# Optimization experiments

Hardware: AMD Instinct MI355X
Metric: run time of the kernel (lower is better)

## Reference

```python
import jax, jax.numpy as jnp
import numpy as np

N = 50000          # nodes
E = 1600000        # edges (avg degree 32)
B = 64             # graphs in batch
D_NODE = 128
D_EDGE = 64
D_EMB = 128
D_HID = 2 * D_EMB  # GCN output channels
EPS = 1e-5


def setup_inputs() -> dict:
    key = jax.random.key(0)
    ks = jax.random.split(key, 12)
    g = lambda k, shape: jax.random.normal(k, shape, jnp.float32) * (shape[0] ** -0.5)
    return {
        "x": jax.random.normal(ks[0], (N, D_NODE), jnp.float32),
        "edge_attr": jax.random.normal(ks[1], (E, D_EDGE), jnp.float32),
        "edge_index": jax.random.randint(ks[2], (2, E), 0, N),
        "batch": jnp.sort(jax.random.randint(ks[3], (N,), 0, B)),
        # GCNConv params
        "W1": g(ks[4], (D_NODE, D_HID)), "b1": jnp.zeros((D_HID,), jnp.float32),
        # TransformerConv params (heads=1)
        "Wq": g(ks[5], (D_HID, D_EMB)), "bq": jnp.zeros((D_EMB,), jnp.float32),
        "Wk": g(ks[6], (D_HID, D_EMB)), "bk": jnp.zeros((D_EMB,), jnp.float32),
        "Wv": g(ks[7], (D_HID, D_EMB)), "bv": jnp.zeros((D_EMB,), jnp.float32),
        "We": g(ks[8], (D_EDGE, D_EMB)), "be": jnp.zeros((D_EMB,), jnp.float32),
        "Wr": g(ks[9], (D_HID, D_EMB)), "br": jnp.zeros((D_EMB,), jnp.float32),
        # LayerNorm params
        "gamma": jnp.ones((D_EMB,), jnp.float32), "beta": jnp.zeros((D_EMB,), jnp.float32),
    }


def _forward(x, edge_attr, edge_index, batch,
             W1, b1, Wq, bq, Wk, bk, Wv, bv, We, be, Wr, br, gamma, beta):
    src, dst = edge_index[0], edge_index[1]

    # ---- GCNConv: symmetric normalization with self-loops ----
    xw = x @ W1                                                # [N, D_HID]
    deg = 1.0 + jax.ops.segment_sum(jnp.ones((E,), x.dtype), dst, num_segments=N)
    dinv = jax.lax.rsqrt(deg)                                  # deg >= 1
    norm = dinv[src] * dinv[dst]                               # [E]
    agg = jax.ops.segment_sum(xw[src] * norm[:, None], dst, num_segments=N)
    h = agg + xw * (dinv * dinv)[:, None] + b1                 # self-loop term
    h = jax.nn.relu(h)                                         # dropout = identity (eval)

    # ---- TransformerConv (heads=1, edge_dim) ----
    q = h @ Wq + bq                                            # [N, D_EMB]
    k = h @ Wk + bk
    v = h @ Wv + bv
    e = edge_attr @ We + be                                    # [E, D_EMB]
    k_j = k[src] + e
    v_j = v[src] + e
    logits = jnp.sum(q[dst] * k_j, axis=-1) / jnp.sqrt(jnp.float32(D_EMB))  # [E]
    # segment softmax over incoming edges of each target node
    lmax = jax.ops.segment_max(logits, dst, num_segments=N)
    exp_l = jnp.exp(logits - lmax[dst])
    denom = jax.ops.segment_sum(exp_l, dst, num_segments=N)
    alpha = exp_l / denom[dst]                                 # [E]
    out = jax.ops.segment_sum(alpha[:, None] * v_j, dst, num_segments=N)
    out = out + h @ Wr + br                                    # root/skip connection

    # ---- LayerNorm + ReLU ----
    mu = jnp.mean(out, axis=-1, keepdims=True)
    var = jnp.var(out, axis=-1, keepdims=True)
    out = (out - mu) * jax.lax.rsqrt(var + EPS) * gamma + beta
    out = jax.nn.relu(out)

    # ---- global mean pool over graphs ----
    sums = jax.ops.segment_sum(out, batch, num_segments=B)     # [B, D_EMB]
    cnts = jax.ops.segment_sum(jnp.ones((N,), out.dtype), batch, num_segments=B)
    return sums / jnp.maximum(cnts, 1.0)[:, None]


def reference(x, edge_attr, edge_index, batch,
              W1, b1, Wq, bq, Wk, bk, Wv, bv, We, be, Wr, br, gamma, beta):
    return _forward(x, edge_attr, edge_index, batch,
                    W1, b1, Wq, bq, Wk, bk, Wv, bv, We, be, Wr, br, gamma, beta)
```

## Files before the change

### kernel.cpp

```cpp
#include <hip/hip_runtime.h>

typedef short bf16x8 __attribute__((ext_vector_type(8)));
typedef float f32x4 __attribute__((ext_vector_type(4)));

#define DN 128
#define DE 64
#define DEMB 128
#define DHID 256
#define SCALE 0.08838834764831845f

__device__ __forceinline__ ushort f2bf(float f) {
  unsigned u = __float_as_uint(f);
  return (ushort)((u + 0x7FFFu + ((u >> 16) & 1u)) >> 16);
}
__device__ __forceinline__ float bf2f(ushort u) {
  return __uint_as_float((unsigned)u << 16);
}

__global__ void k_prep1(const float* __restrict__ W1, ushort* __restrict__ Wp1) {
  int idx = blockIdx.x * 256 + threadIdx.x;
  if (idx >= 16 * 4 * 64 * 8) return;
  int j = idx & 7, lane = (idx >> 3) & 63, s = (idx >> 9) & 3, t = idx >> 11;
  int k = s * 32 + (lane >> 4) * 8 + j;
  int c = t * 16 + (lane & 15);
  Wp1[idx] = f2bf(W1[k * DHID + c]);
}

__global__ void k_prep2(const float* __restrict__ Wq, const float* __restrict__ Wk,
                        const float* __restrict__ Wv, const float* __restrict__ Wr,
                        const float* __restrict__ We, ushort* __restrict__ Wp2) {
  int idx = blockIdx.x * 256 + threadIdx.x;
  if (idx >= 36 * 8 * 64 * 8) return;
  int j = idx & 7, lane = (idx >> 3) & 63, s = (idx >> 9) & 7, t = idx >> 12;
  int k = s * 32 + (lane >> 4) * 8 + j;
  int c = t * 16 + (lane & 15);
  float v;
  if (c < 128)       v = Wq[k * DEMB + c] * SCALE;
  else if (c < 256)  v = Wk[k * DEMB + (c - 128)];
  else if (c < 384)  v = Wv[k * DEMB + (c - 256)];
  else if (c < 512)  v = Wr[k * DEMB + (c - 384)];
  else {
    int cc = c - 512;
    float a = 0.f;
    for (int u = 0; u < DEMB; ++u) a += Wq[k * DEMB + u] * We[cc * DEMB + u];
    v = a * SCALE;
  }
  Wp2[idx] = f2bf(v);
}

__global__ void k_prep_b(const float* __restrict__ bq, const float* __restrict__ bk,
                         const float* __restrict__ bv, const float* __restrict__ br,
                         const float* __restrict__ be, const float* __restrict__ We,
                         float* __restrict__ bcat) {
  int j = blockIdx.x * 256 + threadIdx.x;
  if (j >= 576) return;
  float v;
  if (j < 128)       v = bq[j] * SCALE;
  else if (j < 256)  v = bk[j - 128] + be[j - 128];
  else if (j < 384)  v = bv[j - 256] + be[j - 256];
  else if (j < 512)  v = br[j - 384];
  else {
    int cc = j - 512;
    float a = 0.f;
    for (int u = 0; u < DEMB; ++u) a += bq[u] * We[cc * DEMB + u];
    v = a * SCALE;
  }
  bcat[j] = v;
}

__global__ void k_prep3(const float* __restrict__ We, ushort* __restrict__ Wp3) {
  int idx = blockIdx.x * 256 + threadIdx.x;
  if (idx >= 8 * 2 * 64 * 8) return;
  int j = idx & 7, lane = (idx >> 3) & 63, s = (idx >> 9) & 1, t = idx >> 10;
  int k = s * 32 + (lane >> 4) * 8 + j;
  int c = t * 16 + (lane & 15);
  Wp3[idx] = f2bf(We[k * DEMB + c]);
}

__global__ void k_deg(const int* __restrict__ ei, int* __restrict__ degi, int nE) {
  int e = blockIdx.x * 256 + threadIdx.x;
  if (e < nE) atomicAdd(&degi[ei[nE + e]], 1);
}

__global__ void k_dinv(const int* __restrict__ degi, float* __restrict__ dinv, int nN) {
  int n = blockIdx.x * 256 + threadIdx.x;
  if (n < nN) dinv[n] = rsqrtf(1.0f + (float)degi[n]);
}

__global__ __launch_bounds__(1024) void k_scan(const int* __restrict__ degi,
                                               int* __restrict__ row_ptr, int n) {
  __shared__ int wsum[16];
  __shared__ int carry_s;
  int lane = threadIdx.x & 63, wid = threadIdx.x >> 6;
  if (threadIdx.x == 0) carry_s = 0;
  __syncthreads();
  for (int base = 0; base < n; base += 1024) {
    int i = base + threadIdx.x;
    int v = (i < n) ? degi[i] : 0;
    int sc = v;
    #pragma unroll
    for (int off = 1; off < 64; off <<= 1) {
      int t = __shfl_up(sc, off);
      if (lane >= off) sc += t;
    }
    if (lane == 63) wsum[wid] = sc;
    int carry0 = carry_s;
    __syncthreads();
    if (wid == 0) {
      int w = (lane < 16) ? wsum[lane] : 0;
      int swc = w;
      #pragma unroll
      for (int off = 1; off < 16; off <<= 1) {
        int t = __shfl_up(swc, off);
        if (lane >= off) swc += t;
      }
      if (lane < 16) wsum[lane] = swc - w;
      if (lane == 15) carry_s = carry0 + swc;
    }
    __syncthreads();
    if (i < n) row_ptr[i] = carry0 + wsum[wid] + sc - v;
    __syncthreads();
  }
  if (threadIdx.x == 0) row_ptr[n] = carry_s;
}

__global__ void k_scatter(const int* __restrict__ ei, const int* __restrict__ row_ptr,
                          int* __restrict__ cursor, int2* __restrict__ csr_se, int nE) {
  int e = blockIdx.x * 256 + threadIdx.x;
  if (e >= nE) return;
  int dst = ei[nE + e];
  int pos = row_ptr[dst] + atomicAdd(&cursor[dst], 1);
  csr_se[pos] = make_int2(ei[e], e);
}

__global__ void k_gbounds(const int* __restrict__ batch, int* __restrict__ gstart,
                          int nN, int B) {
  int n = blockIdx.x * 256 + threadIdx.x;
  if (n >= nN) return;
  int b = batch[n];
  if (n == 0) {
    for (int g = 0; g <= b; ++g) gstart[g] = 0;
  } else {
    int pb = batch[n - 1];
    for (int g = pb + 1; g <= b; ++g) gstart[g] = n;
  }
  if (n == nN - 1) {
    for (int g = b + 1; g <= B; ++g) gstart[g] = nN;
  }
}

__global__ __launch_bounds__(256) void k_xcast(const float* __restrict__ x,
                                               const float* __restrict__ dinv,
                                               ushort* __restrict__ xsb, int nN) {
  int idx = blockIdx.x * 256 + threadIdx.x;
  if (idx >= nN * 32) return;
  int n = idx >> 5, q = idx & 31;
  float dn = dinv[n];
  float4 v = *(const float4*)&x[(size_t)n * DN + q * 4];
  ushort4 o;
  o.x = f2bf(v.x * dn); o.y = f2bf(v.y * dn);
  o.z = f2bf(v.z * dn); o.w = f2bf(v.w * dn);
  *(ushort4*)&xsb[(size_t)n * DN + q * 4] = o;
}

__global__ __launch_bounds__(256) void k_gcnX(const ushort* __restrict__ xsb,
                                              const int2* __restrict__ csr_se,
                                              const int* __restrict__ row_ptr,
                                              const float* __restrict__ dinv,
                                              ushort* __restrict__ aggxb, int nN) {
  int lane = threadIdx.x & 63;
  int n = blockIdx.x * 4 + (threadIdx.x >> 6);
  if (n >= nN) return;
  int grp = lane >> 4, l15 = lane & 15;
  int beg = row_ptr[n], end = row_ptr[n + 1];
  float acc[8] = {};
  for (int i0 = beg; i0 < end; i0 += 16) {
    #pragma unroll
    for (int u = 0; u < 4; ++u) {
      int e = i0 + u * 4 + grp;
      bool val = e < end;
      int cl = val ? e : end - 1;
      int src = csr_se[cl].x;
      uint4 xa = *(const uint4*)&xsb[(size_t)src * DN + l15 * 8];
      float w = val ? 1.f : 0.f;
      unsigned qq[4] = {xa.x, xa.y, xa.z, xa.w};
      #pragma unroll
      for (int d = 0; d < 4; ++d) {
        acc[2*d]   = fmaf(w, __uint_as_float(qq[d] << 16), acc[2*d]);
        acc[2*d+1] = fmaf(w, __uint_as_float(qq[d] & 0xFFFF0000u), acc[2*d+1]);
      }
    }
  }
  #pragma unroll
  for (int d = 0; d < 8; ++d) {
    acc[d] += __shfl_xor(acc[d], 16);
    acc[d] += __shfl_xor(acc[d], 32);
  }
  if (grp == 0) {
    uint4 sa = *(const uint4*)&xsb[(size_t)n * DN + l15 * 8];
    unsigned sq[4] = {sa.x, sa.y, sa.z, sa.w};
    float dn = dinv[n];
    ushort o[8];
    #pragma unroll
    for (int d = 0; d < 4; ++d) {
      float lo = __uint_as_float(sq[d] << 16);
      float hi = __uint_as_float(sq[d] & 0xFFFF0000u);
      o[2*d]   = f2bf(dn * (acc[2*d]   + lo));
      o[2*d+1] = f2bf(dn * (acc[2*d+1] + hi));
    }
    uint4 ov = {(unsigned)o[0] | ((unsigned)o[1] << 16),
                (unsigned)o[2] | ((unsigned)o[3] << 16),
                (unsigned)o[4] | ((unsigned)o[5] << 16),
                (unsigned)o[6] | ((unsigned)o[7] << 16)};
    *(uint4*)&aggxb[(size_t)n * DN + l15 * 8] = ov;
  }
}

__global__ __launch_bounds__(256) void k_gemm1b(const ushort* __restrict__ aggxb,
                                                const ushort* __restrict__ Wp1,
                                                const float* __restrict__ b1,
                                                ushort* __restrict__ hb, int nN) {
  int lane = threadIdx.x & 63, wave = threadIdx.x >> 6;
  int l15 = lane & 15, lh = lane >> 4;
  int m0 = blockIdx.x * 16;
  int rowa = m0 + l15; if (rowa >= nN) rowa = nN - 1;
  f32x4 acc[4] = {};
  #pragma unroll
  for (int s = 0; s < 4; ++s) {
    bf16x8 af = *(const bf16x8*)&aggxb[(size_t)rowa * DN + s * 32 + lh * 8];
    #pragma unroll
    for (int tt = 0; tt < 4; ++tt) {
      int t = wave * 4 + tt;
      bf16x8 bf = *(const bf16x8*)&Wp1[((t * 4 + s) * 64 + lane) * 8];
      acc[tt] = __builtin_amdgcn_mfma_f32_16x16x32_bf16(af, bf, acc[tt], 0, 0, 0);
    }
  }
  #pragma unroll
  for (int tt = 0; tt < 4; ++tt) {
    int c = (wave * 4 + tt) * 16 + l15;
    float bc = b1[c];
    #pragma unroll
    for (int r = 0; r < 4; ++r) {
      int row = m0 + lh * 4 + r;
      if (row < nN) hb[(size_t)row * DHID + c] = f2bf(fmaxf(acc[tt][r] + bc, 0.f));
    }
  }
}

__global__ __launch_bounds__(256) void k_gemm2(const ushort* __restrict__ hb,
                                               const ushort* __restrict__ Wp2,
                                               const float* __restrict__ bcat,
                                               ushort* __restrict__ qwb,
                                               ushort* __restrict__ kb,
                                               ushort* __restrict__ vb,
                                               ushort* __restrict__ hrb, int nN) {
  int lane = threadIdx.x & 63, wave = threadIdx.x >> 6;
  int l15 = lane & 15, lh = lane >> 4;
  int m0 = blockIdx.x * 16;
  int rowa = m0 + l15; if (rowa >= nN) rowa = nN - 1;
  f32x4 acc[9] = {};
  for (int s = 0; s < 8; ++s) {
    bf16x8 af = *(const bf16x8*)&hb[(size_t)rowa * DHID + s * 32 + lh * 8];
    #pragma unroll
    for (int tt = 0; tt < 9; ++tt) {
      int t = wave * 9 + tt;
      bf16x8 bf = *(const bf16x8*)&Wp2[((t * 8 + s) * 64 + lane) * 8];
      acc[tt] = __builtin_amdgcn_mfma_f32_16x16x32_bf16(af, bf, acc[tt], 0, 0, 0);
    }
  }
  #pragma unroll
  for (int tt = 0; tt < 9; ++tt) {
    int c = (wave * 9 + tt) * 16 + l15;
    float bc = bcat[c];
    #pragma unroll
    for (int r = 0; r < 4; ++r) {
      int row = m0 + lh * 4 + r;
      if (row >= nN) continue;
      ushort val = f2bf(acc[tt][r] + bc);
      if (c < 128)      qwb[(size_t)row * 192 + c] = val;
      else if (c < 256) kb[(size_t)row * 128 + (c - 128)] = val;
      else if (c < 384) vb[(size_t)row * 128 + (c - 256)] = val;
      else if (c < 512) hrb[(size_t)row * 128 + (c - 384)] = val;
      else              qwb[(size_t)row * 192 + 128 + (c - 512)] = val;
    }
  }
}

__global__ __launch_bounds__(256) void k_edge(const ushort* __restrict__ qwb,
                                              const ushort* __restrict__ kb,
                                              const ushort* __restrict__ vb,
                                              const float* __restrict__ ea32,
                                              const int2* __restrict__ csr_se,
                                              const int* __restrict__ row_ptr,
                                              float* __restrict__ sden,
                                              float* __restrict__ vaccf,
                                              ushort* __restrict__ ewb, int nN) {
  int lane = threadIdx.x & 63;
  int n = blockIdx.x * 4 + (threadIdx.x >> 6);
  if (n >= nN) return;
  int grp = lane >> 4, l15 = lane & 15;
  const ushort* qp = &qwb[(size_t)n * 192];
  bf16x8 qv = *(const bf16x8*)&qp[l15 * 8];
  ushort4 wv = *(const ushort4*)&qp[128 + l15 * 4];
  float q[8];
  #pragma unroll
  for (int d = 0; d < 8; ++d) q[d] = bf2f((ushort)qv[d]);
  float w0 = bf2f(wv.x), w1 = bf2f(wv.y), w2 = bf2f(wv.z), w3 = bf2f(wv.w);
  float s_acc = 0.f;
  float av[8] = {};
  float ae[4] = {};
  int beg = row_ptr[n], end = row_ptr[n + 1];
  for (int i0 = beg; i0 < end; i0 += 16) {
    int2 se[4]; bool vl[4];
    #pragma unroll
    for (int u = 0; u < 4; ++u) {
      int e = i0 + u * 4 + grp;
      vl[u] = e < end;
      se[u] = csr_se[vl[u] ? e : end - 1];
    }
    bf16x8 kv8[4]; bf16x8 vv8[4]; float4 eav[4];
    #pragma unroll
    for (int u = 0; u < 4; ++u) {
      kv8[u] = *(const bf16x8*)&kb[(size_t)se[u].x * 128 + l15 * 8];
      vv8[u] = *(const bf16x8*)&vb[(size_t)se[u].x * 128 + l15 * 8];
      eav[u] = *(const float4*)&ea32[(size_t)se[u].y * DE + l15 * 4];
    }
    #pragma unroll
    for (int u = 0; u < 4; ++u) {
      float dot = w0 * eav[u].x + w1 * eav[u].y + w2 * eav[u].z + w3 * eav[u].w;
      #pragma unroll
      for (int d = 0; d < 8; ++d) dot = fmaf(q[d], bf2f((ushort)kv8[u][d]), dot);
      dot += __shfl_xor(dot, 1);
      dot += __shfl_xor(dot, 2);
      dot += __shfl_xor(dot, 4);
      dot += __shfl_xor(dot, 8);
      float p = vl[u] ? __expf(dot) : 0.f;
      s_acc += p;
      #pragma unroll
      for (int d = 0; d < 8; ++d) av[d] = fmaf(p, bf2f((ushort)vv8[u][d]), av[d]);
      ae[0] = fmaf(p, eav[u].x, ae[0]);
      ae[1] = fmaf(p, eav[u].y, ae[1]);
      ae[2] = fmaf(p, eav[u].z, ae[2]);
      ae[3] = fmaf(p, eav[u].w, ae[3]);
    }
  }
  s_acc += __shfl_xor(s_acc, 16); s_acc += __shfl_xor(s_acc, 32);
  #pragma unroll
  for (int d = 0; d < 8; ++d) {
    av[d] += __shfl_xor(av[d], 16);
    av[d] += __shfl_xor(av[d], 32);
  }
  #pragma unroll
  for (int d = 0; d < 4; ++d) {
    ae[d] += __shfl_xor(ae[d], 16);
    ae[d] += __shfl_xor(ae[d], 32);
  }
  if (grp == 0) {
    if (l15 == 0) sden[n] = s_acc;
    float4 o0 = {av[0], av[1], av[2], av[3]};
    float4 o1 = {av[4], av[5], av[6], av[7]};
    float* vr = &vaccf[(size_t)n * 128 + l15 * 8];
    *(float4*)vr = o0;
    *(float4*)(vr + 4) = o1;
    ushort4 eo;
    eo.x = f2bf(ae[0]); eo.y = f2bf(ae[1]); eo.z = f2bf(ae[2]); eo.w = f2bf(ae[3]);
    *(ushort4*)&ewb[(size_t)n * DE + l15 * 4] = eo;
  }
}

__global__ __launch_bounds__(256) void k_ewe(const ushort* __restrict__ ewb,
                                             const ushort* __restrict__ Wp3,
                                             float* __restrict__ ewout, int nN) {
  int lane = threadIdx.x & 63, wave = threadIdx.x >> 6;
  int l15 = lane & 15, lh = lane >> 4;
  int m0 = blockIdx.x * 16;
  int rowa = m0 + l15; if (rowa >= nN) rowa = nN - 1;
  f32x4 acc[2] = {};
  #pragma unroll
  for (int s = 0; s < 2; ++s) {
    bf16x8 af = *(const bf16x8*)&ewb[(size_t)rowa * DE + s * 32 + lh * 8];
    #pragma unroll
    for (int tt = 0; tt < 2; ++tt) {
      int t = wave * 2 + tt;
      bf16x8 bf = *(const bf16x8*)&Wp3[((t * 2 + s) * 64 + lane) * 8];
      acc[tt] = __builtin_amdgcn_mfma_f32_16x16x32_bf16(af, bf, acc[tt], 0, 0, 0);
    }
  }
  #pragma unroll
  for (int tt = 0; tt < 2; ++tt) {
    int c = (wave * 2 + tt) * 16 + l15;
    #pragma unroll
    for (int r = 0; r < 4; ++r) {
      int row = m0 + lh * 4 + r;
      if (row < nN) ewout[(size_t)row * 128 + c] = acc[tt][r];
    }
  }
}

__global__ __launch_bounds__(256) void k_fin(const float* __restrict__ sden,
                                             const float* __restrict__ vaccf,
                                             const float* __restrict__ ewout,
                                             const ushort* __restrict__ hrb,
                                             const float* __restrict__ gamma,
                                             const float* __restrict__ beta,
                                             float* __restrict__ ynorm, int nN) {
  int lane = threadIdx.x & 63, grp = lane >> 5, l5 = lane & 31;
  int n = blockIdx.x * 8 + (threadIdx.x >> 6) * 2 + grp;
  if (n >= nN) return;
  float s = sden[n];
  float inv = (s > 0.f) ? 1.f / s : 0.f;
  float4 v4 = *(const float4*)&vaccf[(size_t)n * 128 + l5 * 4];
  float4 w4 = *(const float4*)&ewout[(size_t)n * 128 + l5 * 4];
  ushort4 hv = *(const ushort4*)&hrb[(size_t)n * 128 + l5 * 4];
  float4 o4;
  o4.x = (v4.x + w4.x) * inv + bf2f(hv.x);
  o4.y = (v4.y + w4.y) * inv + bf2f(hv.y);
  o4.z = (v4.z + w4.z) * inv + bf2f(hv.z);
  o4.w = (v4.w + w4.w) * inv + bf2f(hv.w);
  float s1 = o4.x + o4.y + o4.z + o4.w;
  float sq = o4.x*o4.x + o4.y*o4.y + o4.z*o4.z + o4.w*o4.w;
  #pragma unroll
  for (int off = 1; off < 32; off <<= 1) {
    s1 += __shfl_xor(s1, off);
    sq += __shfl_xor(sq, off);
  }
  float mu = s1 * (1.f / 128.f);
  float var = sq * (1.f / 128.f) - mu * mu;
  float rstd = rsqrtf(var + 1e-5f);
  float4 g4 = *(const float4*)&gamma[l5 * 4];
  float4 b4 = *(const float4*)&beta[l5 * 4];
  float4 y;
  y.x = fmaxf((o4.x - mu) * rstd * g4.x + b4.x, 0.f);
  y.y = fmaxf((o4.y - mu) * rstd * g4.y + b4.y, 0.f);
  y.z = fmaxf((o4.z - mu) * rstd * g4.z + b4.z, 0.f);
  y.w = fmaxf((o4.w - mu) * rstd * g4.w + b4.w, 0.f);
  *(float4*)&ynorm[(size_t)n * 128 + l5 * 4] = y;
}

__global__ __launch_bounds__(128) void k_pool(const float* __restrict__ ynorm,
                                              const int* __restrict__ gstart,
                                              float* __restrict__ out) {
  int b = blockIdx.x, t = threadIdx.x;
  int beg = gstart[b], end = gstart[b + 1];
  float a0 = 0.f, a1 = 0.f, a2 = 0.f, a3 = 0.f;
  int n = beg;
  for (; n + 4 <= end; n += 4) {
    a0 += ynorm[(size_t)(n + 0) * 128 + t];
    a1 += ynorm[(size_t)(n + 1) * 128 + t];
    a2 += ynorm[(size_t)(n + 2) * 128 + t];
    a3 += ynorm[(size_t)(n + 3) * 128 + t];
  }
  for (; n < end; ++n) a0 += ynorm[(size_t)n * 128 + t];
  float acc = (a0 + a1) + (a2 + a3);
  out[b * 128 + t] = acc / fmaxf((float)(end - beg), 1.f);
}

extern "C" void kernel_launch(void* const* d_in, const int* in_sizes, int n_in,
                              void* d_out, int out_size, void* d_ws, size_t ws_size,
                              hipStream_t stream) {
  const float* x         = (const float*)d_in[0];
  const float* edge_attr = (const float*)d_in[1];
  const int*   edge_index= (const int*)d_in[2];
  const int*   batch     = (const int*)d_in[3];
  const float* W1 = (const float*)d_in[4];
  const float* b1 = (const float*)d_in[5];
  const float* Wq = (const float*)d_in[6];  const float* bq = (const float*)d_in[7];
  const float* Wk = (const float*)d_in[8];  const float* bk = (const float*)d_in[9];
  const float* Wv = (const float*)d_in[10]; const float* bv = (const float*)d_in[11];
  const float* We = (const float*)d_in[12]; const float* be = (const float*)d_in[13];
  const float* Wr = (const float*)d_in[14]; const float* br = (const float*)d_in[15];
  const float* gamma = (const float*)d_in[16];
  const float* beta  = (const float*)d_in[17];
  float* out = (float*)d_out;

  const int nN = in_sizes[0] / DN;
  const int nE = in_sizes[1] / DE;
  const int B  = out_size / DEMB;

  char* p = (char*)d_ws;
  auto alloc = [&](size_t bytes) -> void* {
    void* r = (void*)p;
    p += (bytes + 255) & ~(size_t)255;
    return r;
  };
  int*   degi   = (int*)  alloc((size_t)nN * 4);
  int*   cursor = (int*)  alloc((size_t)nN * 4);
  size_t zero_bytes = (size_t)(p - (char*)d_ws);
  int*    row_ptr = (int*)   alloc((size_t)(nN + 1) * 4);
  int*    gstart  = (int*)   alloc((size_t)(B + 1) * 4);
  float*  dinv    = (float*) alloc((size_t)nN * 4);
  int2*   csr_se  = (int2*)  alloc((size_t)nE * 8);
  ushort* Wp1     = (ushort*)alloc((size_t)16 * 4 * 64 * 8 * 2);
  ushort* Wp2     = (ushort*)alloc((size_t)36 * 8 * 64 * 8 * 2);
  ushort* Wp3     = (ushort*)alloc((size_t)8 * 2 * 64 * 8 * 2);
  float*  bcat    = (float*) alloc(576 * 4);
  ushort* qwb     = (ushort*)alloc((size_t)nN * 192 * 2);
  ushort* hrb     = (ushort*)alloc((size_t)nN * 128 * 2);
  ushort* hb      = (ushort*)alloc((size_t)nN * DHID * 2);
  ushort* xsb     = (ushort*)alloc((size_t)nN * DN * 2);
  ushort* aggxb   = (ushort*)alloc((size_t)nN * DN * 2);
  ushort* kb      = xsb;
  ushort* vb      = aggxb;
  float*  sden    = (float*) alloc((size_t)nN * 4);
  float*  vaccf   = (float*) alloc((size_t)nN * 128 * 4);
  ushort* ewb     = (ushort*)alloc((size_t)nN * DE * 2);
  float*  ewout   = (float*) alloc((size_t)nN * 128 * 4);
  float*  ynorm   = (float*) alloc((size_t)nN * 128 * 4);
  size_t required = (size_t)(p - (char*)d_ws);
  if (ws_size < required) return;

  hipMemsetAsync(d_ws, 0, zero_bytes, stream);

  k_prep1<<<128, 256, 0, stream>>>(W1, Wp1);
  k_prep2<<<576, 256, 0, stream>>>(Wq, Wk, Wv, Wr, We, Wp2);
  k_prep_b<<<3, 256, 0, stream>>>(bq, bk, bv, br, be, We, bcat);
  k_prep3<<<32, 256, 0, stream>>>(We, Wp3);
  k_deg<<<(nE + 255) / 256, 256, 0, stream>>>(edge_index, degi, nE);
  k_dinv<<<(nN + 255) / 256, 256, 0, stream>>>(degi, dinv, nN);
  k_scan<<<1, 1024, 0, stream>>>(degi, row_ptr, nN);
  k_scatter<<<(nE + 255) / 256, 256, 0, stream>>>(edge_index, row_ptr, cursor,
                                                  csr_se, nE);
  k_gbounds<<<(nN + 255) / 256, 256, 0, stream>>>(batch, gstart, nN, B);
  k_xcast<<<(nN * 32 + 255) / 256, 256, 0, stream>>>(x, dinv, xsb, nN);
  k_gcnX<<<(nN + 3) / 4, 256, 0, stream>>>(xsb, csr_se, row_ptr, dinv, aggxb, nN);
  k_gemm1b<<<(nN + 15) / 16, 256, 0, stream>>>(aggxb, Wp1, b1, hb, nN);
  k_gemm2<<<(nN + 15) / 16, 256, 0, stream>>>(hb, Wp2, bcat, qwb, kb, vb, hrb, nN);
  k_edge<<<(nN + 3) / 4, 256, 0, stream>>>(qwb, kb, vb, edge_attr, csr_se, row_ptr,
                                           sden, vaccf, ewb, nN);
  k_ewe<<<(nN + 15) / 16, 256, 0, stream>>>(ewb, Wp3, ewout, nN);
  k_fin<<<(nN + 7) / 8, 256, 0, stream>>>(sden, vaccf, ewout, hrb, gamma, beta,
                                          ynorm, nN);
  k_pool<<<B, 128, 0, stream>>>(ynorm, gstart, out);
}
```

Before: 661.2 us.

## Merge prep/dinv/gbounds kernels and deepen gather batching in gcnX and edge

Folds the four weight-prep kernels into one launch, computes dinv inside the scan kernel, and moves graph-boundary detection into the x-cast kernel, cutting five launches. The GCN aggregation now loads 8 neighbour rows per iteration instead of 4, and the attention edge kernel loads 6 instead of 4, with a launch-bounds occupancy hint. The aim is to reduce launch overhead and expose more memory-level parallelism in the gathers, at the cost of higher register pressure and more wasted lanes on low-degree nodes.

```diff
diff --git a/kernel.cpp b/kernel.cpp
--- a/kernel.cpp
+++ b/kernel.cpp
@@ -17,64 +17,60 @@
   return __uint_as_float((unsigned)u << 16);
 }
 
-__global__ void k_prep1(const float* __restrict__ W1, ushort* __restrict__ Wp1) {
-  int idx = blockIdx.x * 256 + threadIdx.x;
-  if (idx >= 16 * 4 * 64 * 8) return;
-  int j = idx & 7, lane = (idx >> 3) & 63, s = (idx >> 9) & 3, t = idx >> 11;
-  int k = s * 32 + (lane >> 4) * 8 + j;
-  int c = t * 16 + (lane & 15);
-  Wp1[idx] = f2bf(W1[k * DHID + c]);
-}
-
-__global__ void k_prep2(const float* __restrict__ Wq, const float* __restrict__ Wk,
-                        const float* __restrict__ Wv, const float* __restrict__ Wr,
-                        const float* __restrict__ We, ushort* __restrict__ Wp2) {
-  int idx = blockIdx.x * 256 + threadIdx.x;
-  if (idx >= 36 * 8 * 64 * 8) return;
-  int j = idx & 7, lane = (idx >> 3) & 63, s = (idx >> 9) & 7, t = idx >> 12;
-  int k = s * 32 + (lane >> 4) * 8 + j;
-  int c = t * 16 + (lane & 15);
-  float v;
-  if (c < 128)       v = Wq[k * DEMB + c] * SCALE;
-  else if (c < 256)  v = Wk[k * DEMB + (c - 128)];
-  else if (c < 384)  v = Wv[k * DEMB + (c - 256)];
-  else if (c < 512)  v = Wr[k * DEMB + (c - 384)];
-  else {
-    int cc = c - 512;
-    float a = 0.f;
-    for (int u = 0; u < DEMB; ++u) a += Wq[k * DEMB + u] * We[cc * DEMB + u];
-    v = a * SCALE;
-  }
-  Wp2[idx] = f2bf(v);
-}
-
-__global__ void k_prep_b(const float* __restrict__ bq, const float* __restrict__ bk,
-                         const float* __restrict__ bv, const float* __restrict__ br,
-                         const float* __restrict__ be, const float* __restrict__ We,
-                         float* __restrict__ bcat) {
-  int j = blockIdx.x * 256 + threadIdx.x;
-  if (j >= 576) return;
-  float v;
-  if (j < 128)       v = bq[j] * SCALE;
-  else if (j < 256)  v = bk[j - 128] + be[j - 128];
-  else if (j < 384)  v = bv[j - 256] + be[j - 256];
-  else if (j < 512)  v = br[j - 384];
-  else {
-    int cc = j - 512;
-    float a = 0.f;
-    for (int u = 0; u < DEMB; ++u) a += bq[u] * We[cc * DEMB + u];
-    v = a * SCALE;
-  }
-  bcat[j] = v;
-}
-
-__global__ void k_prep3(const float* __restrict__ We, ushort* __restrict__ Wp3) {
-  int idx = blockIdx.x * 256 + threadIdx.x;
-  if (idx >= 8 * 2 * 64 * 8) return;
-  int j = idx & 7, lane = (idx >> 3) & 63, s = (idx >> 9) & 1, t = idx >> 10;
-  int k = s * 32 + (lane >> 4) * 8 + j;
-  int c = t * 16 + (lane & 15);
-  Wp3[idx] = f2bf(We[k * DEMB + c]);
+__global__ void k_prep_all(const float* __restrict__ W1, const float* __restrict__ Wq,
+                           const float* __restrict__ Wk, const float* __restrict__ Wv,
+                           const float* __restrict__ Wr, const float* __restrict__ We,
+                           const float* __restrict__ bq, const float* __restrict__ bk,
+                           const float* __restrict__ bv, const float* __restrict__ br,
+                           const float* __restrict__ be,
+                           ushort* __restrict__ Wp1, ushort* __restrict__ Wp2,
+                           ushort* __restrict__ Wp3, float* __restrict__ bcat) {
+  int bid = blockIdx.x;
+  if (bid < 576) {
+    int idx = bid * 256 + threadIdx.x;
+    int j = idx & 7, lane = (idx >> 3) & 63, s = (idx >> 9) & 7, t = idx >> 12;
+    int k = s * 32 + (lane >> 4) * 8 + j;
+    int c = t * 16 + (lane & 15);
+    float v;
+    if (c < 128)       v = Wq[k * DEMB + c] * SCALE;
+    else if (c < 256)  v = Wk[k * DEMB + (c - 128)];
+    else if (c < 384)  v = Wv[k * DEMB + (c - 256)];
+    else if (c < 512)  v = Wr[k * DEMB + (c - 384)];
+    else {
+      int cc = c - 512;
+      float a = 0.f;
+      for (int u = 0; u < DEMB; ++u) a += Wq[k * DEMB + u] * We[cc * DEMB + u];
+      v = a * SCALE;
+    }
+    Wp2[idx] = f2bf(v);
+  } else if (bid < 704) {
+    int idx = (bid - 576) * 256 + threadIdx.x;
+    int j = idx & 7, lane = (idx >> 3) & 63, s = (idx >> 9) & 3, t = idx >> 11;
+    int k = s * 32 + (lane >> 4) * 8 + j;
+    int c = t * 16 + (lane & 15);
+    Wp1[idx] = f2bf(W1[k * DHID + c]);
+  } else if (bid < 736) {
+    int idx = (bid - 704) * 256 + threadIdx.x;
+    int j = idx & 7, lane = (idx >> 3) & 63, s = (idx >> 9) & 1, t = idx >> 10;
+    int k = s * 32 + (lane >> 4) * 8 + j;
+    int c = t * 16 + (lane & 15);
+    Wp3[idx] = f2bf(We[k * DEMB + c]);
+  } else {
+    int j = (bid - 736) * 256 + threadIdx.x;
+    if (j >= 576) return;
+    float v;
+    if (j < 128)       v = bq[j] * SCALE;
+    else if (j < 256)  v = bk[j - 128] + be[j - 128];
+    else if (j < 384)  v = bv[j - 256] + be[j - 256];
+    else if (j < 512)  v = br[j - 384];
+    else {
+      int cc = j - 512;
+      float a = 0.f;
+      for (int u = 0; u < DEMB; ++u) a += bq[u] * We[cc * DEMB + u];
+      v = a * SCALE;
+    }
+    bcat[j] = v;
+  }
 }
 
 __global__ void k_deg(const int* __restrict__ ei, int* __restrict__ degi, int nE) {
@@ -82,13 +78,9 @@
   if (e < nE) atomicAdd(&degi[ei[nE + e]], 1);
 }
 
-__global__ void k_dinv(const int* __restrict__ degi, float* __restrict__ dinv, int nN) {
-  int n = blockIdx.x * 256 + threadIdx.x;
-  if (n < nN) dinv[n] = rsqrtf(1.0f + (float)degi[n]);
-}
-
 __global__ __launch_bounds__(1024) void k_scan(const int* __restrict__ degi,
-                                               int* __restrict__ row_ptr, int n) {
+                                               int* __restrict__ row_ptr,
+                                               float* __restrict__ dinv, int n) {
   __shared__ int wsum[16];
   __shared__ int carry_s;
   int lane = threadIdx.x & 63, wid = threadIdx.x >> 6;
@@ -97,6 +89,7 @@
   for (int base = 0; base < n; base += 1024) {
     int i = base + threadIdx.x;
     int v = (i < n) ? degi[i] : 0;
+    if (i < n) dinv[i] = rsqrtf(1.0f + (float)v);
     int sc = v;
     #pragma unroll
     for (int off = 1; off < 64; off <<= 1) {
@@ -133,34 +126,33 @@
   csr_se[pos] = make_int2(ei[e], e);
 }
 
-__global__ void k_gbounds(const int* __restrict__ batch, int* __restrict__ gstart,
-                          int nN, int B) {
-  int n = blockIdx.x * 256 + threadIdx.x;
-  if (n >= nN) return;
-  int b = batch[n];
-  if (n == 0) {
-    for (int g = 0; g <= b; ++g) gstart[g] = 0;
-  } else {
-    int pb = batch[n - 1];
-    for (int g = pb + 1; g <= b; ++g) gstart[g] = n;
-  }
-  if (n == nN - 1) {
-    for (int g = b + 1; g <= B; ++g) gstart[g] = nN;
-  }
-}
-
 __global__ __launch_bounds__(256) void k_xcast(const float* __restrict__ x,
                                                const float* __restrict__ dinv,
-                                               ushort* __restrict__ xsb, int nN) {
+                                               const int* __restrict__ batch,
+                                               int* __restrict__ gstart,
+                                               ushort* __restrict__ xsb, int nN, int B) {
   int idx = blockIdx.x * 256 + threadIdx.x;
-  if (idx >= nN * 32) return;
-  int n = idx >> 5, q = idx & 31;
-  float dn = dinv[n];
-  float4 v = *(const float4*)&x[(size_t)n * DN + q * 4];
-  ushort4 o;
-  o.x = f2bf(v.x * dn); o.y = f2bf(v.y * dn);
-  o.z = f2bf(v.z * dn); o.w = f2bf(v.w * dn);
-  *(ushort4*)&xsb[(size_t)n * DN + q * 4] = o;
+  if (idx < nN) {
+    int b = batch[idx];
+    if (idx == 0) {
+      for (int g = 0; g <= b; ++g) gstart[g] = 0;
+    } else {
+      int pb = batch[idx - 1];
+      for (int g = pb + 1; g <= b; ++g) gstart[g] = idx;
+    }
+    if (idx == nN - 1) {
+      for (int g = b + 1; g <= B; ++g) gstart[g] = nN;
+    }
+  }
+  if (idx < nN * 32) {
+    int n = idx >> 5, q = idx & 31;
+    float dn = dinv[n];
+    float4 v = *(const float4*)&x[(size_t)n * DN + q * 4];
+    ushort4 o;
+    o.x = f2bf(v.x * dn); o.y = f2bf(v.y * dn);
+    o.z = f2bf(v.z * dn); o.w = f2bf(v.w * dn);
+    *(ushort4*)&xsb[(size_t)n * DN + q * 4] = o;
+  }
 }
 
 __global__ __launch_bounds__(256) void k_gcnX(const ushort* __restrict__ xsb,
@@ -174,16 +166,22 @@
   int grp = lane >> 4, l15 = lane & 15;
   int beg = row_ptr[n], end = row_ptr[n + 1];
   float acc[8] = {};
-  for (int i0 = beg; i0 < end; i0 += 16) {
-    #pragma unroll
-    for (int u = 0; u < 4; ++u) {
+  for (int i0 = beg; i0 < end; i0 += 32) {
+    int src[8]; bool vl[8];
+    #pragma unroll
+    for (int u = 0; u < 8; ++u) {
       int e = i0 + u * 4 + grp;
-      bool val = e < end;
-      int cl = val ? e : end - 1;
-      int src = csr_se[cl].x;
-      uint4 xa = *(const uint4*)&xsb[(size_t)src * DN + l15 * 8];
-      float w = val ? 1.f : 0.f;
-      unsigned qq[4] = {xa.x, xa.y, xa.z, xa.w};
+      vl[u] = e < end;
+      src[u] = csr_se[vl[u] ? e : end - 1].x;
+    }
+    uint4 xa[8];
+    #pragma unroll
+    for (int u = 0; u < 8; ++u)
+      xa[u] = *(const uint4*)&xsb[(size_t)src[u] * DN + l15 * 8];
+    #pragma unroll
+    for (int u = 0; u < 8; ++u) {
+      float w = vl[u] ? 1.f : 0.f;
+      unsigned qq[4] = {xa[u].x, xa[u].y, xa[u].z, xa[u].w};
       #pragma unroll
       for (int d = 0; d < 4; ++d) {
         acc[2*d]   = fmaf(w, __uint_as_float(qq[d] << 16), acc[2*d]);
@@ -286,15 +284,15 @@
   }
 }
 
-__global__ __launch_bounds__(256) void k_edge(const ushort* __restrict__ qwb,
-                                              const ushort* __restrict__ kb,
-                                              const ushort* __restrict__ vb,
-                                              const float* __restrict__ ea32,
-                                              const int2* __restrict__ csr_se,
-                                              const int* __restrict__ row_ptr,
-                                              float* __restrict__ sden,
-                                              float* __restrict__ vaccf,
-                                              ushort* __restrict__ ewb, int nN) {
+__global__ __launch_bounds__(256, 4) void k_edge(const ushort* __restrict__ qwb,
+                                                 const ushort* __restrict__ kb,
+                                                 const ushort* __restrict__ vb,
+                                                 const float* __restrict__ ea32,
+                                                 const int2* __restrict__ csr_se,
+                                                 const int* __restrict__ row_ptr,
+                                                 float* __restrict__ sden,
+                                                 float* __restrict__ vaccf,
+                                                 ushort* __restrict__ ewb, int nN) {
   int lane = threadIdx.x & 63;
   int n = blockIdx.x * 4 + (threadIdx.x >> 6);
   if (n >= nN) return;
@@ -310,23 +308,23 @@
   float av[8] = {};
   float ae[4] = {};
   int beg = row_ptr[n], end = row_ptr[n + 1];
-  for (int i0 = beg; i0 < end; i0 += 16) {
-    int2 se[4]; bool vl[4];
-    #pragma unroll
-    for (int u = 0; u < 4; ++u) {
+  for (int i0 = beg; i0 < end; i0 += 24) {
+    int2 se[6]; bool vl[6];
+    #pragma unroll
+    for (int u = 0; u < 6; ++u) {
       int e = i0 + u * 4 + grp;
       vl[u] = e < end;
       se[u] = csr_se[vl[u] ? e : end - 1];
     }
-    bf16x8 kv8[4]; bf16x8 vv8[4]; float4 eav[4];
-    #pragma unroll
-    for (int u = 0; u < 4; ++u) {
+    bf16x8 kv8[6]; bf16x8 vv8[6]; float4 eav[6];
+    #pragma unroll
+    for (int u = 0; u < 6; ++u) {
       kv8[u] = *(const bf16x8*)&kb[(size_t)se[u].x * 128 + l15 * 8];
       vv8[u] = *(const bf16x8*)&vb[(size_t)se[u].x * 128 + l15 * 8];
       eav[u] = *(const float4*)&ea32[(size_t)se[u].y * DE + l15 * 4];
     }
     #pragma unroll
-    for (int u = 0; u < 4; ++u) {
+    for (int u = 0; u < 6; ++u) {
       float dot = w0 * eav[u].x + w1 * eav[u].y + w2 * eav[u].z + w3 * eav[u].w;
       #pragma unroll
       for (int d = 0; d < 8; ++d) dot = fmaf(q[d], bf2f((ushort)kv8[u][d]), dot);
@@ -511,17 +509,14 @@
 
   hipMemsetAsync(d_ws, 0, zero_bytes, stream);
 
-  k_prep1<<<128, 256, 0, stream>>>(W1, Wp1);
-  k_prep2<<<576, 256, 0, stream>>>(Wq, Wk, Wv, Wr, We, Wp2);
-  k_prep_b<<<3, 256, 0, stream>>>(bq, bk, bv, br, be, We, bcat);
-  k_prep3<<<32, 256, 0, stream>>>(We, Wp3);
+  k_prep_all<<<739, 256, 0, stream>>>(W1, Wq, Wk, Wv, Wr, We, bq, bk, bv, br, be,
+                                      Wp1, Wp2, Wp3, bcat);
   k_deg<<<(nE + 255) / 256, 256, 0, stream>>>(edge_index, degi, nE);
-  k_dinv<<<(nN + 255) / 256, 256, 0, stream>>>(degi, dinv, nN);
-  k_scan<<<1, 1024, 0, stream>>>(degi, row_ptr, nN);
+  k_scan<<<1, 1024, 0, stream>>>(degi, row_ptr, dinv, nN);
   k_scatter<<<(nE + 255) / 256, 256, 0, stream>>>(edge_index, row_ptr, cursor,
                                                   csr_se, nE);
-  k_gbounds<<<(nN + 255) / 256, 256, 0, stream>>>(batch, gstart, nN, B);
-  k_xcast<<<(nN * 32 + 255) / 256, 256, 0, stream>>>(x, dinv, xsb, nN);
+  k_xcast<<<(nN * 32 + 255) / 256, 256, 0, stream>>>(x, dinv, batch, gstart, xsb,
+                                                     nN, B);
   k_gcnX<<<(nN + 3) / 4, 256, 0, stream>>>(xsb, csr_se, row_ptr, dinv, aggxb, nN);
   k_gemm1b<<<(nN + 15) / 16, 256, 0, stream>>>(aggxb, Wp1, b1, hb, nN);
   k_gemm2<<<(nN + 15) / 16, 256, 0, stream>>>(hb, Wp2, bcat, qwb, kb, vb, hrb, nN);
```

After: 717.8 us. 1.09x slower.
